# Performance work log

Hardware: AMD Instinct MI355X
Metric: run time of the kernel (lower is better)

## Reference

```python
import jax, jax.numpy as jnp
import numpy as np

B, C, H, W = 16, 128, 56, 56
K = 3
F = K * K          # number of deformation filters = kernel taps
OUT = 512
STRIDE = 1


def setup_inputs() -> dict:
    key = jax.random.key(0)
    k1, k2, k3, k4 = jax.random.split(key, 4)
    x = jax.random.normal(k1, (B, C, H, W), jnp.float32)
    # Deform2d 1x1 offset conv: weight [2F, C], bias [2F] initialized to kernel tap offsets
    w_off = jax.random.normal(k2, (2 * F, C), jnp.float32) * 0.01
    half = K // 2
    xs = [float(dx) for dy in range(-half, K - half) for dx in range(-half, K - half)]
    ys = [float(dy) for dy in range(-half, K - half) for dx in range(-half, K - half)]
    b_off = jnp.array(xs + ys, jnp.float32)  # all x offsets first, then all y offsets
    # final 1x1 conv: [OUT, F*C]
    w_conv = jax.random.normal(k3, (OUT, F * C), jnp.float32) * (1.0 / np.sqrt(F * C))
    b_conv = jax.random.normal(k4, (OUT,), jnp.float32) * 0.01
    return {"x": x, "w_off": w_off, "b_off": b_off, "w_conv": w_conv, "b_conv": b_conv}


def _bilinear_sample(img, gx, gy):
    # img: [C,H,W]; gx, gy: [H,W] normalized coords in [-1,1]
    # torch grid_sample defaults: bilinear, zeros padding, align_corners=False
    C_, H_, W_ = img.shape
    ix = ((gx + 1.0) * W_ - 1.0) * 0.5
    iy = ((gy + 1.0) * H_ - 1.0) * 0.5
    x0 = jnp.floor(ix)
    y0 = jnp.floor(iy)
    wx1 = ix - x0
    wx0 = 1.0 - wx1
    wy1 = iy - y0
    wy0 = 1.0 - wy1

    def gather(yy, xx):
        valid = ((xx >= 0) & (xx < W_) & (yy >= 0) & (yy < H_)).astype(img.dtype)
        xi = jnp.clip(xx, 0, W_ - 1).astype(jnp.int32)
        yi = jnp.clip(yy, 0, H_ - 1).astype(jnp.int32)
        return img[:, yi, xi] * valid[None]  # [C,H,W]

    return (gather(y0, x0) * (wy0 * wx0)[None]
            + gather(y0, x0 + 1.0) * (wy0 * wx1)[None]
            + gather(y0 + 1.0, x0) * (wy1 * wx0)[None]
            + gather(y0 + 1.0, x0 + 1.0) * (wy1 * wx1)[None])


def reference(x, w_off, b_off, w_conv, b_conv):
    Bv, Cv, Hv, Wv = x.shape
    scale = 2.0 / max(Hv, Wv)
    # Deform2d: 1x1 conv -> per-pixel offsets, scaled to normalized grid units
    deform = (jnp.einsum('bchw,dc->bdhw', x, w_off) + b_off[None, :, None, None]) * scale
    # matches torch view(B*F, 2, H, W): consecutive channel pairs per filter
    deform = deform.reshape(Bv, F, 2, Hv, Wv)
    # identity grid from affine_grid (align_corners=False)
    base_x = (2.0 * jnp.arange(Wv, dtype=x.dtype) + 1.0) / Wv - 1.0
    base_y = (2.0 * jnp.arange(Hv, dtype=x.dtype) + 1.0) / Hv - 1.0
    # grid is detached in the torch code -> no gradient to the offset conv
    gx = jax.lax.stop_gradient(base_x[None, None, None, :] + deform[:, :, 0])  # [B,F,H,W]
    gy = jax.lax.stop_gradient(base_y[None, None, :, None] + deform[:, :, 1])  # [B,F,H,W]
    sample_f = jax.vmap(_bilinear_sample, in_axes=(None, 0, 0))   # over F filters (input shared)
    sample_bf = jax.vmap(sample_f, in_axes=(0, 0, 0))             # over batch
    sampled = sample_bf(x, gx, gy)                                 # [B,F,C,H,W]
    sampled = sampled.reshape(Bv, F * Cv, Hv, Wv)[:, :, ::STRIDE, ::STRIDE]
    # final 1x1 conv
    return jnp.einsum('bchw,oc->bohw', sampled, w_conv) + b_conv[None, :, None, None]
```

## Files before the change

### kernel.cpp

```cpp
#include <hip/hip_runtime.h>
#include <stdint.h>
#include <stddef.h>

#define BN 16
#define CN 128
#define HN 56
#define WN 56
#define HWN 3136
#define FN 9
#define DN 18
#define ON 512
#define KN 1152
#define MN 50176

typedef __bf16 bf16x8 __attribute__((ext_vector_type(8)));
typedef float f32x4 __attribute__((ext_vector_type(4)));

__device__ __forceinline__ unsigned short f2bf(float f) {
  unsigned int u = __builtin_bit_cast(unsigned int, f);
  u += 0x7fffu + ((u >> 16) & 1u);
  return (unsigned short)(u >> 16);
}

__device__ __forceinline__ void gload_lds16(const void* g, void* l) {
  __builtin_amdgcn_global_load_lds(
      (const __attribute__((address_space(1))) unsigned int*)g,
      (__attribute__((address_space(3))) unsigned int*)l, 16, 0, 0);
}

__global__ void k_transpose(const float* __restrict__ x, unsigned short* __restrict__ xt) {
  __shared__ float tile[32][33];
  const int b = blockIdx.z;
  const int hw0 = blockIdx.x * 32;
  const int c0 = blockIdx.y * 32;
  const int tx = threadIdx.x & 31;
  const int ty = threadIdx.x >> 5;
  const float* xb = x + (size_t)b * CN * HWN;
  unsigned short* xtb = xt + (size_t)b * HWN * CN;
#pragma unroll
  for (int r = 0; r < 4; ++r)
    tile[ty + r * 8][tx] = xb[(size_t)(c0 + ty + r * 8) * HWN + hw0 + tx];
  __syncthreads();
#pragma unroll
  for (int r = 0; r < 4; ++r)
    xtb[(size_t)(hw0 + ty + r * 8) * CN + c0 + tx] = f2bf(tile[tx][ty + r * 8]);
}

__global__ __launch_bounds__(128) void k_prep(const unsigned short* __restrict__ xt,
                                              const float* __restrict__ w_off,
                                              const float* __restrict__ b_off,
                                              const float4* __restrict__ wconv,
                                              ushort4* __restrict__ wb,
                                              float2* __restrict__ ixy) {
  __shared__ __align__(16) char smem[44128];
  const int tid = threadIdx.x;
  if (blockIdx.x >= 392) {
    const int i = (blockIdx.x - 392) * 128 + tid;
    float4 v = wconv[i];
    ushort4 o;
    o.x = f2bf(v.x); o.y = f2bf(v.y); o.z = f2bf(v.z); o.w = f2bf(v.w);
    wb[i] = o;
    return;
  }
  float* lwoff = (float*)(smem + 34816);
  float* lboff = (float*)(smem + 34816 + 9216);
  const int m0 = blockIdx.x * 128;

  const unsigned short* gsrc = xt + (size_t)m0 * CN;
#pragma unroll
  for (int p = 0; p < 16; ++p) {
    const int s = p * 128 + tid;
    uint4 v = *(const uint4*)(gsrc + s * 8);
    *(uint4*)(smem + (s >> 4) * 272 + (s & 15) * 16) = v;
  }
  for (int i = tid; i < DN * CN / 4; i += 128)
    ((float4*)lwoff)[i] = ((const float4*)w_off)[i];
  if (tid < DN) lboff[tid] = b_off[tid];
  __syncthreads();

  const int m = m0 + tid;
  const int b = m / HWN;
  const int hw = m - b * HWN;
  const int h = hw / WN;
  const int w = hw - h * WN;

  float acc[DN];
#pragma unroll
  for (int d = 0; d < DN; ++d) acc[d] = lboff[d];
  const char* rowp = smem + tid * 272;
#pragma unroll
  for (int j = 0; j < 16; ++j) {
    bf16x8 xv = *(const bf16x8*)(rowp + j * 16);
    float xf[8];
#pragma unroll
    for (int q = 0; q < 8; ++q) xf[q] = (float)xv[q];
#pragma unroll
    for (int d = 0; d < DN; ++d) {
      const float* wr = lwoff + d * CN + j * 8;
      acc[d] += xf[0] * wr[0] + xf[1] * wr[1] + xf[2] * wr[2] + xf[3] * wr[3]
              + xf[4] * wr[4] + xf[5] * wr[5] + xf[6] * wr[6] + xf[7] * wr[7];
    }
  }
  const float scale = 2.0f / 56.0f;
  const float bx = (2.0f * w + 1.0f) / (float)WN - 1.0f;
  const float by = (2.0f * h + 1.0f) / (float)HN - 1.0f;
#pragma unroll
  for (int f = 0; f < FN; ++f) {
    float gx = bx + acc[2 * f] * scale;
    float gy = by + acc[2 * f + 1] * scale;
    float ixv = ((gx + 1.0f) * (float)WN - 1.0f) * 0.5f;
    float iyv = ((gy + 1.0f) * (float)HN - 1.0f) * 0.5f;
    ixy[(size_t)m * FN + f] = make_float2(ixv, iyv);
  }
}

__global__ void k_sample(const unsigned short* __restrict__ xt, const float2* __restrict__ ixy,
                         unsigned short* __restrict__ S) {
  const int g = blockIdx.x * 256 + threadIdx.x;
  const int cc = g & 7;
  const int mf = g >> 3;
  const int m = mf / FN;
  const int f = mf - m * FN;
  const int b = m / HWN;

  const float2 p = ixy[mf];
  const float ix = p.x, iy = p.y;
  const float x0f = floorf(ix), y0f = floorf(iy);
  const float wx1 = ix - x0f, wy1 = iy - y0f;
  const float wx0 = 1.0f - wx1, wy0 = 1.0f - wy1;
  const int x0 = (int)x0f, y0 = (int)y0f;
  const int x1 = x0 + 1, y1 = y0 + 1;
  const bool vx0 = (x0 >= 0) & (x0 < WN), vx1 = (x1 >= 0) & (x1 < WN);
  const bool vy0 = (y0 >= 0) & (y0 < HN), vy1 = (y1 >= 0) & (y1 < HN);
  const float w00 = wy0 * wx0 * ((vy0 & vx0) ? 1.0f : 0.0f);
  const float w01 = wy0 * wx1 * ((vy0 & vx1) ? 1.0f : 0.0f);
  const float w10 = wy1 * wx0 * ((vy1 & vx0) ? 1.0f : 0.0f);
  const float w11 = wy1 * wx1 * ((vy1 & vx1) ? 1.0f : 0.0f);
  const int x0c = min(max(x0, 0), WN - 1), x1c = min(max(x1, 0), WN - 1);
  const int y0c = min(max(y0, 0), HN - 1), y1c = min(max(y1, 0), HN - 1);

  const unsigned short* bp = xt + (size_t)b * HWN * CN + cc * 16;
  const bf16x8* p00 = (const bf16x8*)(bp + (size_t)(y0c * WN + x0c) * CN);
  const bf16x8* p01 = (const bf16x8*)(bp + (size_t)(y0c * WN + x1c) * CN);
  const bf16x8* p10 = (const bf16x8*)(bp + (size_t)(y1c * WN + x0c) * CN);
  const bf16x8* p11 = (const bf16x8*)(bp + (size_t)(y1c * WN + x1c) * CN);
  bf16x8 a0 = p00[0], a1 = p00[1];
  bf16x8 b0 = p01[0], b1 = p01[1];
  bf16x8 c0 = p10[0], c1 = p10[1];
  bf16x8 d0 = p11[0], d1 = p11[1];

  unsigned short ov[16];
#pragma unroll
  for (int q = 0; q < 8; ++q) {
    float lo = w00 * (float)a0[q] + w01 * (float)b0[q] + w10 * (float)c0[q] + w11 * (float)d0[q];
    float hi = w00 * (float)a1[q] + w01 * (float)b1[q] + w10 * (float)c1[q] + w11 * (float)d1[q];
    ov[q] = f2bf(lo);
    ov[q + 8] = f2bf(hi);
  }
  uint4* dst = (uint4*)(S + (size_t)m * KN + f * CN + cc * 16);
  dst[0] = *(const uint4*)(ov);
  dst[1] = *(const uint4*)(ov + 8);
}

__global__ __launch_bounds__(256) void k_gemm(const unsigned short* __restrict__ Wb,
                                              const unsigned short* __restrict__ S,
                                              const float* __restrict__ bias,
                                              float* __restrict__ out) {
  __shared__ __align__(16) char smem[32768];
  unsigned short* lw = (unsigned short*)smem;
  unsigned short* ls = (unsigned short*)(smem + 16384);
  const int tid = threadIdx.x;
  const int wave = tid >> 6;
  const int lane = tid & 63;
  const int quad = lane >> 4;
  const int r16 = lane & 15;
  const int bid = blockIdx.x;
  const int ot = (bid >> 3) & 3;
  const int pt = (bid & 7) + ((bid >> 5) << 3);
  const int o0 = ot * 128;
  const int p0 = pt * 128;
  const int wrow = wave >> 1;
  const int wcol = wave & 1;

  f32x4 acc[4][4];
#pragma unroll
  for (int i = 0; i < 4; ++i)
#pragma unroll
    for (int j = 0; j < 4; ++j) acc[i][j] = (f32x4){0.f, 0.f, 0.f, 0.f};

  const int row0 = tid >> 3;
  const int swc = (((tid & 7) ^ (row0 & 7))) * 8;
  const unsigned short* gw = Wb + (size_t)(o0 + row0) * KN + swc;
  const unsigned short* gs = S + (size_t)(p0 + row0) * KN + swc;
  unsigned short* lwd = lw + wave * 512;
  unsigned short* lsd = ls + wave * 512;

  const int rsw = r16 & 7;
  const int ch0 = (quad ^ rsw) * 8;
  const int ch1 = ((quad ^ rsw) ^ 4) * 8;
  const unsigned short* aw = lw + (wrow * 64 + r16) * 64;
  const unsigned short* bs = ls + (wcol * 64 + r16) * 64;

  for (int kt = 0; kt < KN / 64; ++kt) {
#pragma unroll
    for (int r = 0; r < 4; ++r) {
      gload_lds16(gw + (size_t)r * 32 * KN, lwd + r * 2048);
      gload_lds16(gs + (size_t)r * 32 * KN, lsd + r * 2048);
    }
    gw += 64; gs += 64;
    __syncthreads();
#pragma unroll
    for (int h = 0; h < 2; ++h) {
      const int ch = h ? ch1 : ch0;
      bf16x8 afr[4], bfr[4];
#pragma unroll
      for (int i = 0; i < 4; ++i) afr[i] = *(const bf16x8*)(aw + i * 16 * 64 + ch);
#pragma unroll
      for (int j = 0; j < 4; ++j) bfr[j] = *(const bf16x8*)(bs + j * 16 * 64 + ch);
#pragma unroll
      for (int i = 0; i < 4; ++i)
#pragma unroll
        for (int j = 0; j < 4; ++j)
          acc[i][j] = __builtin_amdgcn_mfma_f32_16x16x32_bf16(afr[i], bfr[j], acc[i][j], 0, 0, 0);
    }
    __syncthreads();
  }

  float* lout = (float*)smem;
  for (int half = 0; half < 2; ++half) {
    __syncthreads();
    if (wrow == half) {
#pragma unroll
      for (int i = 0; i < 4; ++i) {
        const int orow = i * 16 + quad * 4;
#pragma unroll
        for (int j = 0; j < 4; ++j) {
          const int col = wcol * 64 + j * 16 + r16;
          lout[(orow + 0) * 128 + col] = acc[i][j][0];
          lout[(orow + 1) * 128 + col] = acc[i][j][1];
          lout[(orow + 2) * 128 + col] = acc[i][j][2];
          lout[(orow + 3) * 128 + col] = acc[i][j][3];
        }
      }
    }
    __syncthreads();
#pragma unroll
    for (int t = 0; t < 8; ++t) {
      const int idx = t * 256 + tid;
      const int orow = idx >> 5;
      const int c4 = idx & 31;
      float4 v = ((const float4*)lout)[idx];
      const int o = o0 + half * 64 + orow;
      const float bv = bias[o];
      v.x += bv; v.y += bv; v.z += bv; v.w += bv;
      const int p = p0 + c4 * 4;
      const int bidx = p / HWN;
      const int hw = p - bidx * HWN;
      *(float4*)(out + (size_t)bidx * ON * HWN + (size_t)o * HWN + hw) = v;
    }
  }
}

extern "C" void kernel_launch(void* const* d_in, const int* in_sizes, int n_in,
                              void* d_out, int out_size, void* d_ws, size_t ws_size,
                              hipStream_t stream) {
  const float* x = (const float*)d_in[0];
  const float* w_off = (const float*)d_in[1];
  const float* b_off = (const float*)d_in[2];
  const float* w_conv = (const float*)d_in[3];
  const float* b_conv = (const float*)d_in[4];
  float* out = (float*)d_out;

  char* ws = (char*)d_ws;
  unsigned short* xt = (unsigned short*)(ws);
  unsigned short* S = (unsigned short*)(ws + 12845056);
  unsigned short* Wb = (unsigned short*)(ws + 128450560);
  float2* ixy = (float2*)(ws + 129630208);

  k_transpose<<<dim3(98, 4, 16), 256, 0, stream>>>(x, xt);
  k_prep<<<dim3(1544), 128, 0, stream>>>(xt, w_off, b_off, (const float4*)w_conv,
                                         (ushort4*)Wb, ixy);
  k_sample<<<dim3(14112), 256, 0, stream>>>(xt, ixy, S);
  k_gemm<<<dim3(1568), 256, 0, stream>>>(Wb, S, b_conv, out);
}
```

Measured before the change: 249.5 us.

## Fuse NCHW-to-NHWC bf16 transpose into offset-conv prep kernel

Removes the standalone transpose kernel. The prep kernel now reads x directly in NCHW layout, coalesced across pixels per channel, and computes the offset conv in fp32 from those values. It also writes the bf16 NHWC copy through shared memory for the sampling stage. This saves one launch and a round trip of the bf16 intermediate, and the offsets now use unrounded fp32 inputs.

Result: no change. 246.4 us (-1.3%).

```diff
diff --git a/kernel.cpp b/kernel.cpp
--- a/kernel.cpp
+++ b/kernel.cpp
@@ -28,31 +28,14 @@
       (__attribute__((address_space(3))) unsigned int*)l, 16, 0, 0);
 }
 
-__global__ void k_transpose(const float* __restrict__ x, unsigned short* __restrict__ xt) {
-  __shared__ float tile[32][33];
-  const int b = blockIdx.z;
-  const int hw0 = blockIdx.x * 32;
-  const int c0 = blockIdx.y * 32;
-  const int tx = threadIdx.x & 31;
-  const int ty = threadIdx.x >> 5;
-  const float* xb = x + (size_t)b * CN * HWN;
-  unsigned short* xtb = xt + (size_t)b * HWN * CN;
-#pragma unroll
-  for (int r = 0; r < 4; ++r)
-    tile[ty + r * 8][tx] = xb[(size_t)(c0 + ty + r * 8) * HWN + hw0 + tx];
-  __syncthreads();
-#pragma unroll
-  for (int r = 0; r < 4; ++r)
-    xtb[(size_t)(hw0 + ty + r * 8) * CN + c0 + tx] = f2bf(tile[tx][ty + r * 8]);
-}
-
-__global__ __launch_bounds__(128) void k_prep(const unsigned short* __restrict__ xt,
-                                              const float* __restrict__ w_off,
-                                              const float* __restrict__ b_off,
-                                              const float4* __restrict__ wconv,
-                                              ushort4* __restrict__ wb,
-                                              float2* __restrict__ ixy) {
-  __shared__ __align__(16) char smem[44128];
+__global__ __launch_bounds__(128) void k_prep2(const float* __restrict__ x,
+                                               const float* __restrict__ w_off,
+                                               const float* __restrict__ b_off,
+                                               const float4* __restrict__ wconv,
+                                               ushort4* __restrict__ wb,
+                                               unsigned short* __restrict__ xt,
+                                               float2* __restrict__ ixy) {
+  __shared__ __align__(16) char smem[44112];
   const int tid = threadIdx.x;
   if (blockIdx.x >= 392) {
     const int i = (blockIdx.x - 392) * 128 + tid;
@@ -63,44 +46,51 @@
     return;
   }
   float* lwoff = (float*)(smem + 34816);
-  float* lboff = (float*)(smem + 34816 + 9216);
+  float* lboff = (float*)(smem + 44032);
   const int m0 = blockIdx.x * 128;
-
-  const unsigned short* gsrc = xt + (size_t)m0 * CN;
-#pragma unroll
-  for (int p = 0; p < 16; ++p) {
-    const int s = p * 128 + tid;
-    uint4 v = *(const uint4*)(gsrc + s * 8);
-    *(uint4*)(smem + (s >> 4) * 272 + (s & 15) * 16) = v;
-  }
+  const int m = m0 + tid;
+  const int bb = m / HWN;
+  const int hw = m - bb * HWN;
+  const int h = hw / WN;
+  const int w = hw - h * WN;
+
   for (int i = tid; i < DN * CN / 4; i += 128)
     ((float4*)lwoff)[i] = ((const float4*)w_off)[i];
   if (tid < DN) lboff[tid] = b_off[tid];
   __syncthreads();
 
-  const int m = m0 + tid;
-  const int b = m / HWN;
-  const int hw = m - b * HWN;
-  const int h = hw / WN;
-  const int w = hw - h * WN;
-
+  const float* xp = x + (size_t)bb * CN * HWN + hw;
   float acc[DN];
 #pragma unroll
   for (int d = 0; d < DN; ++d) acc[d] = lboff[d];
-  const char* rowp = smem + tid * 272;
+
 #pragma unroll
   for (int j = 0; j < 16; ++j) {
-    bf16x8 xv = *(const bf16x8*)(rowp + j * 16);
     float xf[8];
 #pragma unroll
-    for (int q = 0; q < 8; ++q) xf[q] = (float)xv[q];
+    for (int q = 0; q < 8; ++q) xf[q] = xp[(size_t)(j * 8 + q) * HWN];
+    unsigned short ov[8];
+#pragma unroll
+    for (int q = 0; q < 8; ++q) ov[q] = f2bf(xf[q]);
+    *(uint4*)(smem + tid * 272 + j * 16) = *(const uint4*)ov;
 #pragma unroll
     for (int d = 0; d < DN; ++d) {
-      const float* wr = lwoff + d * CN + j * 8;
-      acc[d] += xf[0] * wr[0] + xf[1] * wr[1] + xf[2] * wr[2] + xf[3] * wr[3]
-              + xf[4] * wr[4] + xf[5] * wr[5] + xf[6] * wr[6] + xf[7] * wr[7];
-    }
-  }
+      float4 w0 = *(const float4*)(lwoff + d * CN + j * 8);
+      float4 w1 = *(const float4*)(lwoff + d * CN + j * 8 + 4);
+      acc[d] += xf[0] * w0.x + xf[1] * w0.y + xf[2] * w0.z + xf[3] * w0.w
+              + xf[4] * w1.x + xf[5] * w1.y + xf[6] * w1.z + xf[7] * w1.w;
+    }
+  }
+  __syncthreads();
+
+#pragma unroll
+  for (int p = 0; p < 16; ++p) {
+    const int idx = p * 128 + tid;
+    const int mr = idx >> 4, c16 = idx & 15;
+    uint4 v = *(const uint4*)(smem + mr * 272 + c16 * 16);
+    *(uint4*)(xt + (size_t)(m0 + mr) * CN + c16 * 8) = v;
+  }
+
   const float scale = 2.0f / 56.0f;
   const float bx = (2.0f * w + 1.0f) / (float)WN - 1.0f;
   const float by = (2.0f * h + 1.0f) / (float)HN - 1.0f;
@@ -277,9 +267,8 @@
   unsigned short* Wb = (unsigned short*)(ws + 128450560);
   float2* ixy = (float2*)(ws + 129630208);
 
-  k_transpose<<<dim3(98, 4, 16), 256, 0, stream>>>(x, xt);
-  k_prep<<<dim3(1544), 128, 0, stream>>>(xt, w_off, b_off, (const float4*)w_conv,
-                                         (ushort4*)Wb, ixy);
+  k_prep2<<<dim3(1544), 128, 0, stream>>>(x, w_off, b_off, (const float4*)w_conv,
+                                          (ushort4*)Wb, xt, ixy);
   k_sample<<<dim3(14112), 256, 0, stream>>>(xt, ixy, S);
   k_gemm<<<dim3(1568), 256, 0, stream>>>(Wb, S, b_conv, out);
 }
```
